# Kernel optimization log

Measured on AMD Instinct MI355X. Metric: run time of the kernel, lower is better.

## Reference

```python
import jax, jax.numpy as jnp
import numpy as np

N_NODES = 16384
N_EDGES = 262144
N_GRAPHS = 64
H = 256          # hidden_dim
DE = 192         # edge feature dim
DG = 64          # g_all dim (DE + DG == H)
NITERS = 3


def _lin(key, fan_in, fan_out):
    kw, kb = jax.random.split(key)
    s = 1.0 / np.sqrt(fan_in)
    return (jax.random.uniform(kw, (fan_in, fan_out), jnp.float32, -s, s),
            jax.random.uniform(kb, (fan_out,), jnp.float32, -s, s))


def setup_inputs() -> dict:
    key = jax.random.key(0)
    ks = jax.random.split(key, 12)
    edge_features = jax.random.normal(ks[0], (N_EDGES, DE), jnp.float32)
    g_all = jax.random.normal(ks[1], (1, DG), jnp.float32)
    edge_index = jax.random.randint(ks[2], (2, N_EDGES), 0, N_NODES, jnp.int32)
    # node_degrees: in-degree per node (what the 1/(1+deg) normalization expects)
    node_degrees = jax.ops.segment_sum(jnp.ones((N_EDGES,), jnp.int32), edge_index[1], num_segments=N_NODES)
    # 64 graphs of 256 nodes each (sorted segment ids, no empty graphs)
    batch = jnp.repeat(jnp.arange(N_GRAPHS, dtype=jnp.int32), N_NODES // N_GRAPHS)
    offs = jnp.arange(N_GRAPHS, dtype=jnp.int32) * (N_NODES // N_GRAPHS)
    heads = offs + jax.random.randint(ks[3], (N_GRAPHS,), 0, N_NODES // N_GRAPHS, jnp.int32)
    tails = offs + jax.random.randint(ks[4], (N_GRAPHS,), 0, N_NODES // N_GRAPHS, jnp.int32)
    ea_w1, ea_b1 = _lin(ks[5], H, H)
    ea_w2, ea_b2 = _lin(ks[6], H, 1)
    eu_w1, eu_b1 = _lin(ks[7], 3 * H + 4, H)
    eu_w2, eu_b2 = _lin(ks[8], H, H)
    gw_w1, gw_b1 = _lin(ks[9], 3 * H, H)
    gw_w2, gw_b2 = _lin(ks[10], H, 1)
    ew_w, ew_b = _lin(ks[11], H, 1)
    return dict(edge_features=edge_features, g_all=g_all,
                ea_w1=ea_w1, ea_b1=ea_b1, ea_w2=ea_w2, ea_b2=ea_b2,
                eu_w1=eu_w1, eu_b1=eu_b1, eu_w2=eu_w2, eu_b2=eu_b2,
                gw_w1=gw_w1, gw_b1=gw_b1, gw_w2=gw_w2, gw_b2=gw_b2,
                ew_w=ew_w, ew_b=ew_b,
                edge_index=edge_index, node_degrees=node_degrees,
                batch=batch, heads=heads, tails=tails)


def reference(edge_features, g_all, ea_w1, ea_b1, ea_w2, ea_b2,
              eu_w1, eu_b1, eu_w2, eu_b2, gw_w1, gw_b1, gw_w2, gw_b2,
              ew_w, ew_b, edge_index, node_degrees, batch, heads, tails):
    src, recv = edge_index[0], edge_index[1]
    E = src.shape[0]
    N = node_degrees.shape[0]
    n_graphs = heads.shape[0]
    dt = edge_features.dtype

    # b_e = cat([edge_features, g_all expanded over edges])
    b_e = jnp.concatenate([edge_features, jnp.broadcast_to(g_all, (E, g_all.shape[1]))], axis=1)

    node_ids = jnp.arange(N)
    is_head = (node_ids == heads[batch]).astype(dt)[:, None]
    is_tail = (node_ids == tails[batch]).astype(dt)[:, None]
    deg = node_degrees.astype(dt)[:, None]

    b_v = jnp.zeros((N, b_e.shape[1]), dt)
    for _ in range(NITERS):
        # per-edge attention score
        score = jax.nn.sigmoid(jax.nn.relu(b_e @ ea_w1 + ea_b1) @ ea_w2 + ea_b2)  # [E,1]
        # scatter_softmax over receiver segments
        m = jax.ops.segment_max(score, recv, num_segments=N)
        ex = jnp.exp(score - m[recv])
        s = jax.ops.segment_sum(ex, recv, num_segments=N)
        alpha = ex / s[recv]
        # scatter_add aggregation + degree normalization
        b_v = jax.ops.segment_sum(alpha * b_e, recv, num_segments=N) / (1.0 + deg)  # [N,H]
        # role-augmented node states, gathered back to edges
        r_v = jnp.concatenate([b_v, is_head, is_tail], axis=1)  # [N,H+2]
        msg = jnp.concatenate([r_v[src], r_v[recv], b_e], axis=1)  # [E,3H+4]
        b_e = jax.nn.relu(msg @ eu_w1 + eu_b1) @ eu_w2 + eu_b2  # [E,H]

    g_max = jax.ops.segment_max(b_v, batch, num_segments=n_graphs)  # [G,H]
    g_G = jnp.concatenate([g_max, b_v[heads], b_v[tails]], axis=1)  # [G,3H]
    w_k = jax.nn.softmax(jax.nn.relu(g_G @ gw_w1 + gw_b1) @ gw_w2 + gw_b2, axis=0)  # [G,1]
    g_all_out = jnp.sum(w_k * g_G, axis=0, keepdims=True)  # [1,3H]
    w_e = jax.nn.sigmoid(b_e @ ew_w + ew_b)  # [E,1]
    return (w_e, g_all_out)
```

## Files before the change

kernel.cpp:

```cpp
#include <hip/hip_runtime.h>
#include <stdint.h>

typedef unsigned short u16;
typedef unsigned int   u32;

#define NN 16384
#define NE 262144
#define NG 64
#define HD 256
#define SHS 264

typedef __attribute__((ext_vector_type(8))) short bfrag;
typedef __attribute__((ext_vector_type(4))) float ffrag;

__device__ __forceinline__ float bf2f(u16 h){
  union { u32 u; float f; } v; v.u = ((u32)h) << 16; return v.f;
}
__device__ __forceinline__ u16 f2bf(float x){
  union { float f; u32 u; } v; v.f = x;
  u32 r = v.u + 0x7fffu + ((v.u >> 16) & 1u);
  return (u16)(r >> 16);
}
__device__ __forceinline__ float sigmoidf(float x){ return 1.f/(1.f+__expf(-x)); }

__device__ __forceinline__ void dma16(const void* g, void* l){
  __builtin_amdgcn_global_load_lds(
      (const __attribute__((address_space(1))) u32*)g,
      (__attribute__((address_space(3))) u32*)l, 16, 0, 0);
}


enum { MODE_SCORE=0, MODE_PQ=4 };

template<int MODE>
__global__ __launch_bounds__(256, 4)
void gemm_k(const u16* __restrict__ A, const u16* __restrict__ Bf0,
            const u16* __restrict__ Bf1,
            float* __restrict__ outF, u16* __restrict__ out0, u16* __restrict__ out1,
            const float* __restrict__ bias, const float* __restrict__ vec,
            const float* __restrict__ scal, const float* __restrict__ flags,
            const float* __restrict__ ht0, const float* __restrict__ ht1)
{
  __shared__ __align__(16) u16 sA[16384];
  __shared__ float sred[4][64];

  const int l  = threadIdx.x & 63;
  const int w  = threadIdx.x >> 6;
  const int q  = l >> 4;
  const int ml = l & 15;
  const long rowBase = (long)blockIdx.x * 64;

  const u16* Bf   = Bf0;
  u16*       outB = out0;
  const float* htp = ht0;
  const float* bp  = bias;
  if (MODE==MODE_PQ && blockIdx.y){ Bf = Bf1; outB = out1; htp = ht1; bp = nullptr; }

  const u16* gA = A + (size_t)(rowBase + w*16 + ml)*HD + q*8;
#pragma unroll
  for (int c=0; c<8; ++c) dma16(gA + c*32, sA + (c*4+w)*512);

  ffrag acc[4][4];
  if constexpr (MODE==MODE_SCORE){
#pragma unroll
    for (int n=0; n<4; ++n){
      const float bb = bias[(w*4+n)*16+ml];
#pragma unroll
      for (int mt=0; mt<4; ++mt) acc[mt][n] = (ffrag){bb,bb,bb,bb};
    }
  } else {
    float h0[4], h1[4], bb[4];
#pragma unroll
    for (int n=0; n<4; ++n){
      const int col = (w*4+n)*16+ml;
      h0[n] = htp[col]; h1[n] = htp[HD+col]; bb[n] = bp ? bp[col] : 0.f;
    }
    float2 fl[16];
#pragma unroll
    for (int i=0; i<16; ++i){
      long row = rowBase + (i>>2)*16 + q*4 + (i&3);
      fl[i] = *(const float2*)(flags + 2*row);
    }
#pragma unroll
    for (int i=0; i<16; ++i){
      const int mt = i>>2, r = i&3;
      const float fh = fl[i].x, ft = fl[i].y;
#pragma unroll
      for (int n=0; n<4; ++n)
        acc[mt][n][r] = bb[n] + fh*h0[n] + ft*h1[n];
    }
  }
  __syncthreads();

#pragma unroll 1
  for (int c=0; c<8; ++c){
    bfrag a[4], b[4];
#pragma unroll
    for (int n=0; n<4; ++n)
      b[n] = *(const bfrag*)(Bf + (((size_t)c*16 + w*4 + n)*64 + l)*8);
#pragma unroll
    for (int mt=0; mt<4; ++mt) a[mt] = *(const bfrag*)(sA + (c*4+mt)*512 + l*8);
#pragma unroll
    for (int mt=0; mt<4; ++mt)
#pragma unroll
      for (int n=0; n<4; ++n)
        acc[mt][n] = __builtin_amdgcn_mfma_f32_16x16x32_bf16(a[mt], b[n], acc[mt][n], 0, 0, 0);
  }

  if constexpr (MODE==MODE_SCORE){
    float part[4][4];
#pragma unroll
    for (int mt=0; mt<4; ++mt)
#pragma unroll
      for (int r=0; r<4; ++r) part[mt][r] = 0.f;
#pragma unroll
    for (int n=0; n<4; ++n){
      const float vvn = vec[(w*4+n)*16+ml];
#pragma unroll
      for (int mt=0; mt<4; ++mt)
#pragma unroll
        for (int r=0; r<4; ++r)
          part[mt][r] += fmaxf(acc[mt][n][r], 0.f) * vvn;
    }
#pragma unroll
    for (int mt=0; mt<4; ++mt)
#pragma unroll
      for (int r=0; r<4; ++r){
        float p = part[mt][r];
        p += __shfl_xor(p, 1, 64); p += __shfl_xor(p, 2, 64);
        p += __shfl_xor(p, 4, 64); p += __shfl_xor(p, 8, 64);
        part[mt][r] = p;
      }
    if (ml == 0)
#pragma unroll
      for (int mt=0; mt<4; ++mt)
#pragma unroll
        for (int r=0; r<4; ++r)
          sred[w][mt*16 + q*4 + r] = part[mt][r];
    __syncthreads();
    if (threadIdx.x < 64){
      const int t = threadIdx.x;
      float v = sred[0][t] + sred[1][t] + sred[2][t] + sred[3][t];
      outF[rowBase + t] = sigmoidf(v + scal[0]);
    }
  } else {
#pragma unroll
    for (int mt=0; mt<4; ++mt)
#pragma unroll
      for (int r=0; r<4; ++r){
        long row = rowBase + mt*16 + q*4 + r;
        u16 o[4];
#pragma unroll
        for (int n=0; n<4; ++n) o[n] = f2bf(acc[mt][n][r]);
        uint2 pk; pk.x = (u32)o[0] | ((u32)o[1]<<16); pk.y = (u32)o[2] | ((u32)o[3]<<16);
        *(uint2*)(outB + (size_t)row*HD + w*64 + ml*4) = pk;
      }
  }
}

template<bool LAST>
__global__ __launch_bounds__(256, 4)
void mega_k(u16* __restrict__ BE, const u16* __restrict__ w1cf,
            const u16* __restrict__ w2f, const u16* __restrict__ eaw1f,
            float* __restrict__ scoreOut, float* __restrict__ weOut,
            const u16* __restrict__ Pg, const u16* __restrict__ Qg,
            const int* __restrict__ srcI, const int* __restrict__ recvI,
            const float* __restrict__ b2,
            const float* __restrict__ sb1, const float* __restrict__ sv,
            const float* __restrict__ ssc,
            const float* __restrict__ wv, const float* __restrict__ wb)
{
  __shared__ __align__(16) u16 sU[64*SHS];
  __shared__ float sred[4][64];

  const int l  = threadIdx.x & 63;
  const int w  = threadIdx.x >> 6;
  const int q  = l >> 4;
  const int ml = l & 15;
  const long rowBase = (long)blockIdx.x * 64;

  const u16* gA = BE + (size_t)(rowBase + w*16 + ml)*HD + q*8;
#pragma unroll
  for (int c=0; c<8; ++c) dma16(gA + c*32, sU + (c*4+w)*512);
  __syncthreads();

  ffrag acc[4][4];
#pragma unroll
  for (int mt=0; mt<4; ++mt)
#pragma unroll
    for (int n=0; n<4; ++n) acc[mt][n] = (ffrag){0.f,0.f,0.f,0.f};

#pragma unroll 1
  for (int c=0; c<8; ++c){
    bfrag a[4], b[4];
#pragma unroll
    for (int n=0; n<4; ++n)
      b[n] = *(const bfrag*)(w1cf + (((size_t)c*16 + w*4 + n)*64 + l)*8);
#pragma unroll
    for (int mt=0; mt<4; ++mt) a[mt] = *(const bfrag*)(sU + (c*4+mt)*512 + l*8);
#pragma unroll
    for (int mt=0; mt<4; ++mt)
#pragma unroll
      for (int n=0; n<4; ++n)
        acc[mt][n] = __builtin_amdgcn_mfma_f32_16x16x32_bf16(a[mt], b[n], acc[mt][n], 0, 0, 0);
  }
  __syncthreads();

#pragma unroll
  for (int mt=0; mt<4; ++mt)
#pragma unroll
    for (int r=0; r<4; ++r){
      long row = rowBase + mt*16 + q*4 + r;
      const int si = srcI[row];
      const int ri = recvI[row];
      uint2 pu = *(const uint2*)(Pg + (size_t)si*HD + w*64 + ml*4);
      uint2 qu = *(const uint2*)(Qg + (size_t)ri*HD + w*64 + ml*4);
      u16 o[4];
      float pv[4] = { bf2f((u16)(pu.x & 0xffff)), bf2f((u16)(pu.x >> 16)),
                      bf2f((u16)(pu.y & 0xffff)), bf2f((u16)(pu.y >> 16)) };
      float qv[4] = { bf2f((u16)(qu.x & 0xffff)), bf2f((u16)(qu.x >> 16)),
                      bf2f((u16)(qu.y & 0xffff)), bf2f((u16)(qu.y >> 16)) };
#pragma unroll
      for (int n=0; n<4; ++n)
        o[n] = f2bf(fmaxf(acc[mt][n][r] + pv[n] + qv[n], 0.f));
      uint2 pk; pk.x = (u32)o[0] | ((u32)o[1]<<16); pk.y = (u32)o[2] | ((u32)o[3]<<16);
      *(uint2*)(sU + (size_t)(mt*16 + q*4 + r)*SHS + w*64 + ml*4) = pk;
    }
  __syncthreads();

#pragma unroll
  for (int mt=0; mt<4; ++mt)
#pragma unroll
    for (int n=0; n<4; ++n) acc[mt][n] = (ffrag){0.f,0.f,0.f,0.f};
#pragma unroll 1
  for (int c=0; c<8; ++c){
    bfrag a[4], b[4];
#pragma unroll
    for (int n=0; n<4; ++n)
      b[n] = *(const bfrag*)(w2f + (((size_t)c*16 + w*4 + n)*64 + l)*8);
#pragma unroll
    for (int mt=0; mt<4; ++mt)
      a[mt] = *(const bfrag*)(sU + (size_t)(mt*16+ml)*SHS + c*32 + q*8);
#pragma unroll
    for (int mt=0; mt<4; ++mt)
#pragma unroll
      for (int n=0; n<4; ++n)
        acc[mt][n] = __builtin_amdgcn_mfma_f32_16x16x32_bf16(a[mt], b[n], acc[mt][n], 0, 0, 0);
  }

  float bia2[4];
#pragma unroll
  for (int n=0; n<4; ++n) bia2[n] = b2[(w*4+n)*16+ml];

  if constexpr (!LAST){
    __syncthreads();
#pragma unroll
    for (int mt=0; mt<4; ++mt)
#pragma unroll
      for (int r=0; r<4; ++r){
        long row = rowBase + mt*16 + q*4 + r;
        u16 o[4];
#pragma unroll
        for (int n=0; n<4; ++n) o[n] = f2bf(acc[mt][n][r] + bia2[n]);
        uint2 pk; pk.x = (u32)o[0] | ((u32)o[1]<<16); pk.y = (u32)o[2] | ((u32)o[3]<<16);
        *(uint2*)(BE + (size_t)row*HD + w*64 + ml*4) = pk;
        *(uint2*)(sU + (size_t)(mt*16 + q*4 + r)*SHS + w*64 + ml*4) = pk;
      }
    __syncthreads();

#pragma unroll
    for (int mt=0; mt<4; ++mt)
#pragma unroll
      for (int n=0; n<4; ++n) acc[mt][n] = (ffrag){0.f,0.f,0.f,0.f};
#pragma unroll 1
    for (int c=0; c<8; ++c){
      bfrag a[4], b[4];
#pragma unroll
      for (int n=0; n<4; ++n)
        b[n] = *(const bfrag*)(eaw1f + (((size_t)c*16 + w*4 + n)*64 + l)*8);
#pragma unroll
      for (int mt=0; mt<4; ++mt)
        a[mt] = *(const bfrag*)(sU + (size_t)(mt*16+ml)*SHS + c*32 + q*8);
#pragma unroll
      for (int mt=0; mt<4; ++mt)
#pragma unroll
        for (int n=0; n<4; ++n)
          acc[mt][n] = __builtin_amdgcn_mfma_f32_16x16x32_bf16(a[mt], b[n], acc[mt][n], 0, 0, 0);
    }
    float part[4][4];
#pragma unroll
    for (int mt=0; mt<4; ++mt)
#pragma unroll
      for (int r=0; r<4; ++r) part[mt][r] = 0.f;
#pragma unroll
    for (int n=0; n<4; ++n){
      const int col = (w*4+n)*16+ml;
      const float bb = sb1[col], vvn = sv[col];
#pragma unroll
      for (int mt=0; mt<4; ++mt)
#pragma unroll
        for (int r=0; r<4; ++r)
          part[mt][r] += fmaxf(acc[mt][n][r] + bb, 0.f) * vvn;
    }
#pragma unroll
    for (int mt=0; mt<4; ++mt)
#pragma unroll
      for (int r=0; r<4; ++r){
        float p = part[mt][r];
        p += __shfl_xor(p, 1, 64); p += __shfl_xor(p, 2, 64);
        p += __shfl_xor(p, 4, 64); p += __shfl_xor(p, 8, 64);
        part[mt][r] = p;
      }
    if (ml == 0)
#pragma unroll
      for (int mt=0; mt<4; ++mt)
#pragma unroll
        for (int r=0; r<4; ++r)
          sred[w][mt*16 + q*4 + r] = part[mt][r];
    __syncthreads();
    if (threadIdx.x < 64){
      const int t = threadIdx.x;
      float v = sred[0][t] + sred[1][t] + sred[2][t] + sred[3][t];
      scoreOut[rowBase + t] = sigmoidf(v + ssc[0]);
    }
  } else {
    float part[4][4];
#pragma unroll
    for (int mt=0; mt<4; ++mt)
#pragma unroll
      for (int r=0; r<4; ++r) part[mt][r] = 0.f;
#pragma unroll
    for (int n=0; n<4; ++n){
      const float vvn = wv[(w*4+n)*16+ml];
#pragma unroll
      for (int mt=0; mt<4; ++mt)
#pragma unroll
        for (int r=0; r<4; ++r)
          part[mt][r] += (acc[mt][n][r] + bia2[n]) * vvn;
    }
#pragma unroll
    for (int mt=0; mt<4; ++mt)
#pragma unroll
      for (int r=0; r<4; ++r){
        float p = part[mt][r];
        p += __shfl_xor(p, 1, 64); p += __shfl_xor(p, 2, 64);
        p += __shfl_xor(p, 4, 64); p += __shfl_xor(p, 8, 64);
        part[mt][r] = p;
      }
    if (ml == 0)
#pragma unroll
      for (int mt=0; mt<4; ++mt)
#pragma unroll
        for (int r=0; r<4; ++r)
          sred[w][mt*16 + q*4 + r] = part[mt][r];
    __syncthreads();
    if (threadIdx.x < 64){
      const int t = threadIdx.x;
      float v = sred[0][t] + sred[1][t] + sred[2][t] + sred[3][t];
      weOut[rowBase + t] = sigmoidf(v + wb[0]);
    }
  }
}

__global__ void repack_k(const float* __restrict__ B, u16* __restrict__ out){
  int t = blockIdx.x*256 + threadIdx.x;
  int l = t & 63, n = (t>>6)&15, c = t>>10;
  int col = n*16 + (l&15);
  int kbase = c*32 + ((l>>4)<<3);
#pragma unroll
  for (int j=0; j<8; ++j){
    int kp = kbase + j;
    int f = (kp>>6)*64 + (kp&3)*16 + ((kp>>2)&15);
    out[(size_t)t*8 + j] = f2bf(B[(size_t)f*HD + col]);
  }
}

__global__ void initbe_k(const float* __restrict__ ef, const float* __restrict__ gall,
                         u16* __restrict__ BE){
  int t = blockIdx.x*256 + threadIdx.x;
  int e = t >> 6; int p4 = (t & 63) * 4;
  int w64 = p4 >> 6, mlr = (p4 >> 2) & 15;
  u16 o[4];
#pragma unroll
  for (int i=0; i<4; ++i){
    int f = w64*64 + i*16 + mlr;
    float v = (f < 192) ? ef[(size_t)e*192 + f] : gall[f - 192];
    o[i] = f2bf(v);
  }
  uint2 pk; pk.x = (u32)o[0] | ((u32)o[1]<<16); pk.y = (u32)o[2] | ((u32)o[3]<<16);
  *(uint2*)(BE + (size_t)e*HD + p4) = pk;
}

__global__ void flags_k(const int* __restrict__ batch, const int* __restrict__ heads,
                        const int* __restrict__ tails, float* __restrict__ flags){
  int n = blockIdx.x*256 + threadIdx.x;
  int g = batch[n];
  flags[2*n]   = (n == heads[g]) ? 1.f : 0.f;
  flags[2*n+1] = (n == tails[g]) ? 1.f : 0.f;
}

__global__ void scan_k(const int* __restrict__ deg, int* __restrict__ offs,
                       int* __restrict__ cur){
  __shared__ int part[256];
  int tid = threadIdx.x;
  int base = tid * 64;
  int s = 0;
  for (int j=0; j<64; ++j) s += deg[base+j];
  part[tid] = s;
  __syncthreads();
  if (tid == 0){
    int run = 0;
    for (int i=0; i<256; ++i){ int t = part[i]; part[i] = run; run += t; }
  }
  __syncthreads();
  int run = part[tid];
  for (int j=0; j<64; ++j){
    offs[base+j] = run; cur[base+j] = run; run += deg[base+j];
  }
  if (tid == 255) offs[NN] = run;
}

__global__ void fill_k(const int* __restrict__ recv, int* __restrict__ cur,
                       int* __restrict__ eids){
  int e = blockIdx.x*256 + threadIdx.x;
  int r = recv[e];
  int p = atomicAdd(&cur[r], 1);
  eids[p] = e;
}

__global__ __launch_bounds__(256)
void agg_k(const float* __restrict__ score, const u16* __restrict__ BE,
           const int* __restrict__ offs, const int* __restrict__ eids,
           float* __restrict__ bv, u16* __restrict__ bvb){
  int node = blockIdx.x*4 + (threadIdx.x >> 6);
  int l = threadIdx.x & 63;
  int beg = offs[node], end = offs[node+1];

  float m = -1e30f;
  for (int i=beg+l; i<end; i+=64) m = fmaxf(m, score[eids[i]]);
#pragma unroll
  for (int d=1; d<64; d<<=1) m = fmaxf(m, __shfl_xor(m, d, 64));

  float s = 0.f;
  for (int i=beg+l; i<end; i+=64) s += __expf(score[eids[i]] - m);
#pragma unroll
  for (int d=1; d<64; d<<=1) s += __shfl_xor(s, d, 64);

  float deg = (float)(end - beg);
  float scale = (end > beg) ? (1.f/s) * (1.f/(1.f+deg)) : 0.f;

  float a0=0.f, a1=0.f, a2=0.f, a3=0.f;
  for (int i=beg; i<end; ++i){
    int e = eids[i];
    float al = __expf(score[e] - m);
    uint2 uv = *(const uint2*)(BE + (size_t)e*HD + l*4);
    a0 += al * bf2f((u16)(uv.x & 0xffff));
    a1 += al * bf2f((u16)(uv.x >> 16));
    a2 += al * bf2f((u16)(uv.y & 0xffff));
    a3 += al * bf2f((u16)(uv.y >> 16));
  }
  size_t o = (size_t)node*HD + l*4;
  a0 *= scale; a1 *= scale; a2 *= scale; a3 *= scale;
  bv[o+0]=a0; bv[o+1]=a1; bv[o+2]=a2; bv[o+3]=a3;
  uint2 p; p.x = (u32)f2bf(a0) | ((u32)f2bf(a1)<<16);
  p.y = (u32)f2bf(a2) | ((u32)f2bf(a3)<<16);
  *(uint2*)(bvb + o) = p;
}

__global__ void gmax_k(const float* __restrict__ bv, const int* __restrict__ heads,
                       const int* __restrict__ tails, float* __restrict__ gG){
  int g = blockIdx.x, col = threadIdx.x;
  float mx = -1e30f;
  const float* p = bv + (size_t)g*256*HD + col;
  for (int i=0; i<256; ++i) mx = fmaxf(mx, p[(size_t)i*HD]);
  gG[g*768 + col]       = mx;
  gG[g*768 + 256 + col] = bv[(size_t)heads[g]*HD + col];
  gG[g*768 + 512 + col] = bv[(size_t)tails[g]*HD + col];
}

__global__ void glog_k(const float* __restrict__ gG, const float* __restrict__ w1,
                       const float* __restrict__ b1, const float* __restrict__ w2,
                       const float* __restrict__ b2, float* __restrict__ logits){
  int g = blockIdx.x, n = threadIdx.x;
  float a = b1[n];
  const float* gg = gG + g*768;
  for (int k=0; k<768; ++k){
    int b = k >> 8, p = k & 255;
    int f = (p>>6)*64 + (p&3)*16 + ((p>>2)&15);
    a += gg[k] * w1[(size_t)(b*256 + f)*HD + n];
  }
  a = fmaxf(a, 0.f) * w2[n];
#pragma unroll
  for (int d=1; d<64; d<<=1) a += __shfl_xor(a, d, 64);
  __shared__ float red[4];
  if ((threadIdx.x & 63) == 0) red[threadIdx.x >> 6] = a;
  __syncthreads();
  if (threadIdx.x == 0) logits[g] = red[0]+red[1]+red[2]+red[3] + b2[0];
}

__global__ void gfin_k(const float* __restrict__ gG, const float* __restrict__ logits,
                       float* __restrict__ out){
  int tid = threadIdx.x;
  float m = -1e30f;
  for (int g=0; g<NG; ++g) m = fmaxf(m, logits[g]);
  float s = 0.f;
  for (int g=0; g<NG; ++g) s += __expf(logits[g] - m);
  float inv = 1.f/s;
  for (int j=tid; j<768; j+=256){
    int b = j >> 8, f = j & 255;
    int p = (f>>6)*64 + (f&15)*4 + ((f>>4)&3);
    float o = 0.f;
    for (int g=0; g<NG; ++g) o += __expf(logits[g]-m)*inv * gG[g*768 + b*256 + p];
    out[j] = o;
  }
}

extern "C" void kernel_launch(void* const* d_in, const int* in_sizes, int n_in,
                              void* d_out, int out_size, void* d_ws, size_t ws_size,
                              hipStream_t stream)
{
  const float* ef    = (const float*)d_in[0];
  const float* gall  = (const float*)d_in[1];
  const float* ea_w1 = (const float*)d_in[2];
  const float* ea_b1 = (const float*)d_in[3];
  const float* ea_w2 = (const float*)d_in[4];
  const float* ea_b2 = (const float*)d_in[5];
  const float* eu_w1 = (const float*)d_in[6];
  const float* eu_b1 = (const float*)d_in[7];
  const float* eu_w2 = (const float*)d_in[8];
  const float* eu_b2 = (const float*)d_in[9];
  const float* gw_w1 = (const float*)d_in[10];
  const float* gw_b1 = (const float*)d_in[11];
  const float* gw_w2 = (const float*)d_in[12];
  const float* gw_b2 = (const float*)d_in[13];
  const float* ew_w  = (const float*)d_in[14];
  const float* ew_b  = (const float*)d_in[15];
  const int* eidx    = (const int*)d_in[16];
  const int* srcI    = eidx;
  const int* recvI   = eidx + NE;
  const int* ndeg    = (const int*)d_in[17];
  const int* batch   = (const int*)d_in[18];
  const int* heads   = (const int*)d_in[19];
  const int* tails   = (const int*)d_in[20];
  float* out = (float*)d_out;

  char* wsb = (char*)d_ws;
  size_t off = 0;
  auto alloc = [&](size_t sz)->char*{
    char* p = wsb + off; off = (off + sz + 255) & ~(size_t)255; return p;
  };
  u16*   BE    = (u16*)  alloc((size_t)NE*HD*2);
  float* score = (float*)alloc((size_t)NE*4);
  u16*   P     = (u16*)  alloc((size_t)NN*HD*2);
  u16*   Q     = (u16*)  alloc((size_t)NN*HD*2);
  float* bv    = (float*)alloc((size_t)NN*HD*4);
  u16*   bvb   = (u16*)  alloc((size_t)NN*HD*2);
  int*   offs  = (int*)  alloc((size_t)(NN+1)*4);
  int*   cur   = (int*)  alloc((size_t)NN*4);
  int*   eids  = (int*)  alloc((size_t)NE*4);
  float* flags = (float*)alloc((size_t)NN*8);
  u16*   eaw1f = (u16*)  alloc((size_t)65536*2);
  u16*   w1af  = (u16*)  alloc((size_t)65536*2);
  u16*   w1bf  = (u16*)  alloc((size_t)65536*2);
  u16*   w1cf  = (u16*)  alloc((size_t)65536*2);
  u16*   euw2f = (u16*)  alloc((size_t)65536*2);
  float* gG    = (float*)alloc((size_t)NG*768*4);
  float* logits= (float*)alloc((size_t)NG*4);

  repack_k<<<32,256,0,stream>>>(ea_w1, eaw1f);
  repack_k<<<32,256,0,stream>>>(eu_w1, w1af);
  repack_k<<<32,256,0,stream>>>(eu_w1 + 258*HD, w1bf);
  repack_k<<<32,256,0,stream>>>(eu_w1 + 516*HD, w1cf);
  repack_k<<<32,256,0,stream>>>(eu_w2, euw2f);
  initbe_k<<<NE*64/256,256,0,stream>>>(ef, gall, BE);
  flags_k<<<NN/256,256,0,stream>>>(batch, heads, tails, flags);
  scan_k<<<1,256,0,stream>>>(ndeg, offs, cur);
  fill_k<<<NE/256,256,0,stream>>>(recvI, cur, eids);

  gemm_k<MODE_SCORE><<<NE/64,256,0,stream>>>(BE, eaw1f, nullptr, score,
      nullptr, nullptr, ea_b1, ea_w2, ea_b2, nullptr, nullptr, nullptr);

  for (int it=0; it<3; ++it){
    agg_k<<<NN/4,256,0,stream>>>(score, BE, offs, eids, bv, bvb);
    gemm_k<MODE_PQ><<<dim3(NN/64,2),256,0,stream>>>(bvb, w1af, w1bf, nullptr,
        P, Q, eu_b1, nullptr, nullptr, flags, eu_w1 + 256*HD, eu_w1 + 514*HD);
    if (it < 2){
      mega_k<false><<<NE/64,256,0,stream>>>(BE, w1cf, euw2f, eaw1f,
          score, nullptr, P, Q, srcI, recvI, eu_b2,
          ea_b1, ea_w2, ea_b2, nullptr, nullptr);
    } else {
      mega_k<true><<<NE/64,256,0,stream>>>(BE, w1cf, euw2f, eaw1f,
          nullptr, out, P, Q, srcI, recvI, eu_b2,
          nullptr, nullptr, nullptr, ew_w, ew_b);
    }
  }

  gmax_k<<<NG,256,0,stream>>>(bv, heads, tails, gG);
  glog_k<<<NG,256,0,stream>>>(gG, gw_w1, gw_b1, gw_w2, gw_b2, logits);
  gfin_k<<<1,256,0,stream>>>(gG, logits, out + NE);
}
```

Baseline: 998.2 us.

## Retile edge mega-kernel to 128-row blocks with 8 waves

The fused edge-update kernel now processes 128 edges per block with 512 threads. Each wave covers 32 output columns across all 8 row tiles, instead of 64 columns across 4 row tiles. This halves how often weight fragments are reloaded per edge, since each B fragment is reused over more rows. In exchange, LDS reads of A fragments per MFMA rise, the P/Q gathers shrink to 4-byte accesses, and the larger shared-memory footprint may lower the number of resident blocks.

```diff
diff --git a/kernel.cpp b/kernel.cpp
--- a/kernel.cpp
+++ b/kernel.cpp
@@ -159,7 +159,7 @@
 }
 
 template<bool LAST>
-__global__ __launch_bounds__(256, 4)
+__global__ __launch_bounds__(512, 4)
 void mega_k(u16* __restrict__ BE, const u16* __restrict__ w1cf,
             const u16* __restrict__ w2f, const u16* __restrict__ eaw1f,
             float* __restrict__ scoreOut, float* __restrict__ weOut,
@@ -170,193 +170,172 @@
             const float* __restrict__ ssc,
             const float* __restrict__ wv, const float* __restrict__ wb)
 {
-  __shared__ __align__(16) u16 sU[64*SHS];
-  __shared__ float sred[4][64];
+  __shared__ __align__(16) u16 sU[128*SHS];
+  __shared__ float sred[8][128];
 
   const int l  = threadIdx.x & 63;
   const int w  = threadIdx.x >> 6;
   const int q  = l >> 4;
   const int ml = l & 15;
-  const long rowBase = (long)blockIdx.x * 64;
+  const long rowBase = (long)blockIdx.x * 128;
+
+  const int ppb = (w>>1)*64 + ml*4 + (w&1)*2;
 
   const u16* gA = BE + (size_t)(rowBase + w*16 + ml)*HD + q*8;
 #pragma unroll
-  for (int c=0; c<8; ++c) dma16(gA + c*32, sU + (c*4+w)*512);
-  __syncthreads();
-
-  ffrag acc[4][4];
-#pragma unroll
-  for (int mt=0; mt<4; ++mt)
-#pragma unroll
-    for (int n=0; n<4; ++n) acc[mt][n] = (ffrag){0.f,0.f,0.f,0.f};
+  for (int c=0; c<8; ++c) dma16(gA + c*32, sU + (c*8+w)*512);
+  __syncthreads();
+
+  ffrag acc[8][2];
+#pragma unroll
+  for (int g=0; g<8; ++g){
+    acc[g][0] = (ffrag){0.f,0.f,0.f,0.f};
+    acc[g][1] = (ffrag){0.f,0.f,0.f,0.f};
+  }
 
 #pragma unroll 1
   for (int c=0; c<8; ++c){
-    bfrag a[4], b[4];
-#pragma unroll
-    for (int n=0; n<4; ++n)
-      b[n] = *(const bfrag*)(w1cf + (((size_t)c*16 + w*4 + n)*64 + l)*8);
-#pragma unroll
-    for (int mt=0; mt<4; ++mt) a[mt] = *(const bfrag*)(sU + (c*4+mt)*512 + l*8);
-#pragma unroll
-    for (int mt=0; mt<4; ++mt)
-#pragma unroll
-      for (int n=0; n<4; ++n)
-        acc[mt][n] = __builtin_amdgcn_mfma_f32_16x16x32_bf16(a[mt], b[n], acc[mt][n], 0, 0, 0);
-  }
-  __syncthreads();
-
-#pragma unroll
-  for (int mt=0; mt<4; ++mt)
+    bfrag b0 = *(const bfrag*)(w1cf + (((size_t)c*16 + w*2 + 0)*64 + l)*8);
+    bfrag b1 = *(const bfrag*)(w1cf + (((size_t)c*16 + w*2 + 1)*64 + l)*8);
+#pragma unroll
+    for (int g=0; g<8; ++g){
+      bfrag a = *(const bfrag*)(sU + (c*8+g)*512 + l*8);
+      acc[g][0] = __builtin_amdgcn_mfma_f32_16x16x32_bf16(a, b0, acc[g][0], 0, 0, 0);
+      acc[g][1] = __builtin_amdgcn_mfma_f32_16x16x32_bf16(a, b1, acc[g][1], 0, 0, 0);
+    }
+  }
+  __syncthreads();
+
+#pragma unroll
+  for (int g=0; g<8; ++g)
 #pragma unroll
     for (int r=0; r<4; ++r){
-      long row = rowBase + mt*16 + q*4 + r;
+      const int rl = g*16 + q*4 + r;
+      const long row = rowBase + rl;
       const int si = srcI[row];
       const int ri = recvI[row];
-      uint2 pu = *(const uint2*)(Pg + (size_t)si*HD + w*64 + ml*4);
-      uint2 qu = *(const uint2*)(Qg + (size_t)ri*HD + w*64 + ml*4);
-      u16 o[4];
-      float pv[4] = { bf2f((u16)(pu.x & 0xffff)), bf2f((u16)(pu.x >> 16)),
-                      bf2f((u16)(pu.y & 0xffff)), bf2f((u16)(pu.y >> 16)) };
-      float qv[4] = { bf2f((u16)(qu.x & 0xffff)), bf2f((u16)(qu.x >> 16)),
-                      bf2f((u16)(qu.y & 0xffff)), bf2f((u16)(qu.y >> 16)) };
-#pragma unroll
-      for (int n=0; n<4; ++n)
-        o[n] = f2bf(fmaxf(acc[mt][n][r] + pv[n] + qv[n], 0.f));
-      uint2 pk; pk.x = (u32)o[0] | ((u32)o[1]<<16); pk.y = (u32)o[2] | ((u32)o[3]<<16);
-      *(uint2*)(sU + (size_t)(mt*16 + q*4 + r)*SHS + w*64 + ml*4) = pk;
-    }
-  __syncthreads();
-
-#pragma unroll
-  for (int mt=0; mt<4; ++mt)
-#pragma unroll
-    for (int n=0; n<4; ++n) acc[mt][n] = (ffrag){0.f,0.f,0.f,0.f};
+      u32 pu = *(const u32*)(Pg + (size_t)si*HD + ppb);
+      u32 qu = *(const u32*)(Qg + (size_t)ri*HD + ppb);
+      u16 o0 = f2bf(fmaxf(acc[g][0][r] + bf2f((u16)(pu & 0xffff)) + bf2f((u16)(qu & 0xffff)), 0.f));
+      u16 o1 = f2bf(fmaxf(acc[g][1][r] + bf2f((u16)(pu >> 16))    + bf2f((u16)(qu >> 16)),    0.f));
+      *(u32*)(sU + (size_t)rl*SHS + ppb) = (u32)o0 | ((u32)o1<<16);
+    }
+  __syncthreads();
+
+#pragma unroll
+  for (int g=0; g<8; ++g){
+    acc[g][0] = (ffrag){0.f,0.f,0.f,0.f};
+    acc[g][1] = (ffrag){0.f,0.f,0.f,0.f};
+  }
 #pragma unroll 1
   for (int c=0; c<8; ++c){
-    bfrag a[4], b[4];
-#pragma unroll
-    for (int n=0; n<4; ++n)
-      b[n] = *(const bfrag*)(w2f + (((size_t)c*16 + w*4 + n)*64 + l)*8);
-#pragma unroll
-    for (int mt=0; mt<4; ++mt)
-      a[mt] = *(const bfrag*)(sU + (size_t)(mt*16+ml)*SHS + c*32 + q*8);
-#pragma unroll
-    for (int mt=0; mt<4; ++mt)
-#pragma unroll
-      for (int n=0; n<4; ++n)
-        acc[mt][n] = __builtin_amdgcn_mfma_f32_16x16x32_bf16(a[mt], b[n], acc[mt][n], 0, 0, 0);
-  }
-
-  float bia2[4];
-#pragma unroll
-  for (int n=0; n<4; ++n) bia2[n] = b2[(w*4+n)*16+ml];
+    bfrag b0 = *(const bfrag*)(w2f + (((size_t)c*16 + w*2 + 0)*64 + l)*8);
+    bfrag b1 = *(const bfrag*)(w2f + (((size_t)c*16 + w*2 + 1)*64 + l)*8);
+#pragma unroll
+    for (int g=0; g<8; ++g){
+      bfrag a = *(const bfrag*)(sU + (size_t)(g*16+ml)*SHS + c*32 + q*8);
+      acc[g][0] = __builtin_amdgcn_mfma_f32_16x16x32_bf16(a, b0, acc[g][0], 0, 0, 0);
+      acc[g][1] = __builtin_amdgcn_mfma_f32_16x16x32_bf16(a, b1, acc[g][1], 0, 0, 0);
+    }
+  }
+
+  const float bia20 = b2[(w*2+0)*16+ml];
+  const float bia21 = b2[(w*2+1)*16+ml];
 
   if constexpr (!LAST){
     __syncthreads();
 #pragma unroll
-    for (int mt=0; mt<4; ++mt)
+    for (int g=0; g<8; ++g)
 #pragma unroll
       for (int r=0; r<4; ++r){
-        long row = rowBase + mt*16 + q*4 + r;
-        u16 o[4];
-#pragma unroll
-        for (int n=0; n<4; ++n) o[n] = f2bf(acc[mt][n][r] + bia2[n]);
-        uint2 pk; pk.x = (u32)o[0] | ((u32)o[1]<<16); pk.y = (u32)o[2] | ((u32)o[3]<<16);
-        *(uint2*)(BE + (size_t)row*HD + w*64 + ml*4) = pk;
-        *(uint2*)(sU + (size_t)(mt*16 + q*4 + r)*SHS + w*64 + ml*4) = pk;
+        const int rl = g*16 + q*4 + r;
+        const long row = rowBase + rl;
+        u16 o0 = f2bf(acc[g][0][r] + bia20);
+        u16 o1 = f2bf(acc[g][1][r] + bia21);
+        u32 pk = (u32)o0 | ((u32)o1<<16);
+        *(u32*)(BE + (size_t)row*HD + ppb) = pk;
+        *(u32*)(sU + (size_t)rl*SHS + ppb) = pk;
       }
     __syncthreads();
 
 #pragma unroll
-    for (int mt=0; mt<4; ++mt)
-#pragma unroll
-      for (int n=0; n<4; ++n) acc[mt][n] = (ffrag){0.f,0.f,0.f,0.f};
+    for (int g=0; g<8; ++g){
+      acc[g][0] = (ffrag){0.f,0.f,0.f,0.f};
+      acc[g][1] = (ffrag){0.f,0.f,0.f,0.f};
+    }
 #pragma unroll 1
     for (int c=0; c<8; ++c){
-      bfrag a[4], b[4];
-#pragma unroll
-      for (int n=0; n<4; ++n)
-        b[n] = *(const bfrag*)(eaw1f + (((size_t)c*16 + w*4 + n)*64 + l)*8);
-#pragma unroll
-      for (int mt=0; mt<4; ++mt)
-        a[mt] = *(const bfrag*)(sU + (size_t)(mt*16+ml)*SHS + c*32 + q*8);
-#pragma unroll
-      for (int mt=0; mt<4; ++mt)
-#pragma unroll
-        for (int n=0; n<4; ++n)
-          acc[mt][n] = __builtin_amdgcn_mfma_f32_16x16x32_bf16(a[mt], b[n], acc[mt][n], 0, 0, 0);
-    }
-    float part[4][4];
-#pragma unroll
-    for (int mt=0; mt<4; ++mt)
-#pragma unroll
-      for (int r=0; r<4; ++r) part[mt][r] = 0.f;
-#pragma unroll
-    for (int n=0; n<4; ++n){
-      const int col = (w*4+n)*16+ml;
-      const float bb = sb1[col], vvn = sv[col];
-#pragma unroll
-      for (int mt=0; mt<4; ++mt)
-#pragma unroll
-        for (int r=0; r<4; ++r)
-          part[mt][r] += fmaxf(acc[mt][n][r] + bb, 0.f) * vvn;
-    }
-#pragma unroll
-    for (int mt=0; mt<4; ++mt)
+      bfrag b0 = *(const bfrag*)(eaw1f + (((size_t)c*16 + w*2 + 0)*64 + l)*8);
+      bfrag b1 = *(const bfrag*)(eaw1f + (((size_t)c*16 + w*2 + 1)*64 + l)*8);
+#pragma unroll
+      for (int g=0; g<8; ++g){
+        bfrag a = *(const bfrag*)(sU + (size_t)(g*16+ml)*SHS + c*32 + q*8);
+        acc[g][0] = __builtin_amdgcn_mfma_f32_16x16x32_bf16(a, b0, acc[g][0], 0, 0, 0);
+        acc[g][1] = __builtin_amdgcn_mfma_f32_16x16x32_bf16(a, b1, acc[g][1], 0, 0, 0);
+      }
+    }
+    const float sb0 = sb1[(w*2+0)*16+ml], sv0 = sv[(w*2+0)*16+ml];
+    const float sb1v = sb1[(w*2+1)*16+ml], sv1 = sv[(w*2+1)*16+ml];
+    float part[8][4];
+#pragma unroll
+    for (int g=0; g<8; ++g)
+#pragma unroll
+      for (int r=0; r<4; ++r)
+        part[g][r] = fmaxf(acc[g][0][r] + sb0, 0.f) * sv0
+                   + fmaxf(acc[g][1][r] + sb1v, 0.f) * sv1;
+#pragma unroll
+    for (int g=0; g<8; ++g)
 #pragma unroll
       for (int r=0; r<4; ++r){
-        float p = part[mt][r];
+        float p = part[g][r];
         p += __shfl_xor(p, 1, 64); p += __shfl_xor(p, 2, 64);
         p += __shfl_xor(p, 4, 64); p += __shfl_xor(p, 8, 64);
-        part[mt][r] = p;
+        part[g][r] = p;
       }
     if (ml == 0)
 #pragma unroll
-      for (int mt=0; mt<4; ++mt)
+      for (int g=0; g<8; ++g)
 #pragma unroll
         for (int r=0; r<4; ++r)
-          sred[w][mt*16 + q*4 + r] = part[mt][r];
+          sred[w][g*16 + q*4 + r] = part[g][r];
     __syncthreads();
-    if (threadIdx.x < 64){
+    if (threadIdx.x < 128){
       const int t = threadIdx.x;
-      float v = sred[0][t] + sred[1][t] + sred[2][t] + sred[3][t];
+      float v = 0.f;
+#pragma unroll
+      for (int ww=0; ww<8; ++ww) v += sred[ww][t];
       scoreOut[rowBase + t] = sigmoidf(v + ssc[0]);
     }
   } else {
-    float part[4][4];
-#pragma unroll
-    for (int mt=0; mt<4; ++mt)
-#pragma unroll
-      for (int r=0; r<4; ++r) part[mt][r] = 0.f;
-#pragma unroll
-    for (int n=0; n<4; ++n){
-      const float vvn = wv[(w*4+n)*16+ml];
-#pragma unroll
-      for (int mt=0; mt<4; ++mt)
-#pragma unroll
-        for (int r=0; r<4; ++r)
-          part[mt][r] += (acc[mt][n][r] + bia2[n]) * vvn;
-    }
-#pragma unroll
-    for (int mt=0; mt<4; ++mt)
+    const float wv0 = wv[(w*2+0)*16+ml];
+    const float wv1 = wv[(w*2+1)*16+ml];
+    float part[8][4];
+#pragma unroll
+    for (int g=0; g<8; ++g)
+#pragma unroll
+      for (int r=0; r<4; ++r)
+        part[g][r] = (acc[g][0][r] + bia20) * wv0 + (acc[g][1][r] + bia21) * wv1;
+#pragma unroll
+    for (int g=0; g<8; ++g)
 #pragma unroll
       for (int r=0; r<4; ++r){
-        float p = part[mt][r];
+        float p = part[g][r];
         p += __shfl_xor(p, 1, 64); p += __shfl_xor(p, 2, 64);
         p += __shfl_xor(p, 4, 64); p += __shfl_xor(p, 8, 64);
-        part[mt][r] = p;
+        part[g][r] = p;
       }
     if (ml == 0)
 #pragma unroll
-      for (int mt=0; mt<4; ++mt)
+      for (int g=0; g<8; ++g)
 #pragma unroll
         for (int r=0; r<4; ++r)
-          sred[w][mt*16 + q*4 + r] = part[mt][r];
+          sred[w][g*16 + q*4 + r] = part[g][r];
     __syncthreads();
-    if (threadIdx.x < 64){
+    if (threadIdx.x < 128){
       const int t = threadIdx.x;
-      float v = sred[0][t] + sred[1][t] + sred[2][t] + sred[3][t];
+      float v = 0.f;
+#pragma unroll
+      for (int ww=0; ww<8; ++ww) v += sred[ww][t];
       weOut[rowBase + t] = sigmoidf(v + wb[0]);
     }
   }
@@ -585,11 +564,11 @@
     gemm_k<MODE_PQ><<<dim3(NN/64,2),256,0,stream>>>(bvb, w1af, w1bf, nullptr,
         P, Q, eu_b1, nullptr, nullptr, flags, eu_w1 + 256*HD, eu_w1 + 514*HD);
     if (it < 2){
-      mega_k<false><<<NE/64,256,0,stream>>>(BE, w1cf, euw2f, eaw1f,
+      mega_k<false><<<NE/128,512,0,stream>>>(BE, w1cf, euw2f, eaw1f,
           score, nullptr, P, Q, srcI, recvI, eu_b2,
           ea_b1, ea_w2, ea_b2, nullptr, nullptr);
     } else {
-      mega_k<true><<<NE/64,256,0,stream>>>(BE, w1cf, euw2f, eaw1f,
+      mega_k<true><<<NE/128,512,0,stream>>>(BE, w1cf, euw2f, eaw1f,
           nullptr, out, P, Q, srcI, recvI, eu_b2,
           nullptr, nullptr, nullptr, ew_w, ew_b);
     }
```

New measurement: 1.101 ms. +10.3%, slower.
